# Kernel tuning notes

Hardware: AMD Instinct MI355X
Metric: run time of the kernel (lower is better)

## Reference

```python
import jax, jax.numpy as jnp
import numpy as np

GROUPS = 4
GROUP_SIZE = 64
NORMED = True


def setup_inputs() -> dict:
    key = jax.random.key(0)
    k1, k2 = jax.random.split(key)
    x = jax.random.normal(k1, (2, 4096, 4096), dtype=jnp.float32)
    # weight: [groups*group_out, group_in] = [4096, 1024], init std 0.02 as in torch
    weight = jax.random.normal(k2, (4096, 1024), dtype=jnp.float32) * 0.02
    return {"x": x, "weight": weight}


def reference(x, weight):
    if NORMED:
        # F.rms_norm with eps=None uses finfo(dtype).eps
        eps = jnp.finfo(x.dtype).eps
        x = x * jax.lax.rsqrt(jnp.mean(x * x, axis=-1, keepdims=True) + eps)

    # bf16 cast of weight (matches torch `.bfloat16()`), quantize in flat chunks of GROUP_SIZE
    w = weight.astype(jnp.bfloat16)
    w_g = w.reshape(-1, GROUP_SIZE)
    scale = jnp.clip(jnp.mean(jnp.abs(w_g), axis=-1, keepdims=True), 1e-8, None)
    q = jnp.clip(jnp.round(w_g / scale), -1.0, 1.0)
    # STE: forward value is q*scale, gradient flows through w
    w_ternary = w + jax.lax.stop_gradient((q * scale).reshape(w.shape) - w)

    group_in = weight.shape[1]
    group_out = weight.shape[0] // GROUPS
    w_grouped = w_ternary.reshape(GROUPS, group_out, group_in)

    bsz = x.shape[:-1]
    x_g = x.reshape(bsz + (GROUPS, group_in))
    # block-diagonal grouped matmul; promote bf16 weight to x dtype (exact upcast)
    out = jnp.einsum('...gi,goi->...go', x_g, w_grouped.astype(x.dtype))
    return out.reshape(bsz + (GROUPS * group_out,))
```

## Files before the change

kernel.cpp:

```cpp
#include <hip/hip_runtime.h>
#include <hip/hip_bf16.h>
#include <stdint.h>

__device__ __forceinline__ unsigned short f2bf(float f) {
    __hip_bfloat16 h = __float2bfloat16(f);
    return *reinterpret_cast<unsigned short*>(&h);
}
__device__ __forceinline__ float bf2f(unsigned short u) {
    __hip_bfloat16 h = *reinterpret_cast<__hip_bfloat16*>(&u);
    return __bfloat162float(h);
}

typedef __attribute__((ext_vector_type(8))) short bf16x8;
typedef __attribute__((ext_vector_type(4))) float f32x4;

__device__ __forceinline__ void async16(const void* g, void* l) {
    __builtin_amdgcn_global_load_lds(
        (const __attribute__((address_space(1))) unsigned int*)g,
        (__attribute__((address_space(3))) unsigned int*)l,
        16, 0, 0);
}

__global__ __launch_bounds__(256) void quant_kernel(const float* __restrict__ W,
                                                    unsigned short* __restrict__ Wq) {
    int idx = blockIdx.x * 256 + threadIdx.x;
    float wf = W[idx];
    float wbf = bf2f(f2bf(wf));
    float a = fabsf(wbf);
    float s = a;
    #pragma unroll
    for (int off = 32; off; off >>= 1) s += __shfl_xor(s, off, 64);
    float mean = s * (1.0f / 64.0f);
    float sf = bf2f(f2bf(mean));
    sf = fmaxf(sf, 1.0011718e-08f);
    float quot = bf2f(f2bf(wbf / sf));
    float q = rintf(quot);
    q = fminf(1.0f, fmaxf(-1.0f, q));
    float qs = q * sf;
    float d  = bf2f(f2bf(qs - wbf));
    Wq[idx] = f2bf(wbf + d);
}

__global__ __launch_bounds__(256) void norm_kernel(const float* __restrict__ X,
                                                   unsigned short* __restrict__ Xb) {
    __shared__ float red[4];
    const long long row = blockIdx.x;
    const float4* xr = (const float4*)(X + row * 4096);
    const int t = threadIdx.x;
    float4 v[4];
    float ss = 0.f;
    #pragma unroll
    for (int i = 0; i < 4; ++i) {
        v[i] = xr[i * 256 + t];
        ss += v[i].x * v[i].x + v[i].y * v[i].y + v[i].z * v[i].z + v[i].w * v[i].w;
    }
    #pragma unroll
    for (int off = 32; off; off >>= 1) ss += __shfl_xor(ss, off, 64);
    if ((t & 63) == 0) red[t >> 6] = ss;
    __syncthreads();
    const float tot = red[0] + red[1] + red[2] + red[3];
    const float scale = 1.0f / sqrtf(tot * (1.0f / 4096.0f) + 1.1920928955078125e-07f);
    ushort4* ob = (ushort4*)(Xb + row * 4096);
    #pragma unroll
    for (int i = 0; i < 4; ++i) {
        ushort4 o;
        o.x = f2bf(v[i].x * scale);
        o.y = f2bf(v[i].y * scale);
        o.z = f2bf(v[i].z * scale);
        o.w = f2bf(v[i].w * scale);
        ob[i * 256 + t] = o;
    }
}

__global__ __launch_bounds__(512, 2) void gemm_kernel(const unsigned short* __restrict__ Xb,
                                                      const unsigned short* __restrict__ Wq,
                                                      float* __restrict__ Out) {
    __shared__ unsigned short lsA[4][256 * 32];
    __shared__ unsigned short lsB[4][256 * 32];

    const int tid = threadIdx.x;
    const int lane = tid & 63;
    const int wv = tid >> 6;
    const int wr = wv >> 2;
    const int wc = wv & 3;

    const int bid = blockIdx.x;
    const int swz = (bid & 7) * 64 + (bid >> 3);
    const int bm0 = (swz & 31) * 256;
    const int bn0 = (swz >> 5) * 256;
    const int g = bn0 >> 10;

    const int srow = tid >> 2;
    const int cswz = (tid & 3) ^ ((tid >> 3) & 3);
    const unsigned short* pA0 = Xb + (long long)(bm0 + srow) * 4096 + g * 1024 + cswz * 8;
    const unsigned short* pA1 = pA0 + (long long)128 * 4096;
    const unsigned short* pB0 = Wq + (long long)(bn0 + srow) * 1024 + cswz * 8;
    const unsigned short* pB1 = pB0 + (long long)128 * 1024;
    const int ldst = tid * 8;

    const int cb = (lane >> 4) ^ ((lane >> 1) & 3);
    const int aOff = (wr * 128 + (lane & 15)) * 32 + cb * 8;
    const int bOff = (wc * 64 + (lane & 15)) * 32 + cb * 8;

    f32x4 acc[8][4];
    #pragma unroll
    for (int i = 0; i < 8; ++i)
        #pragma unroll
        for (int j = 0; j < 4; ++j) acc[i][j] = (f32x4){0.f, 0.f, 0.f, 0.f};

    const int T = 32;

    #pragma unroll
    for (int pt = 0; pt < 3; ++pt) {
        async16(pA0 + pt * 32, &lsA[pt][ldst]);
        async16(pA1 + pt * 32, &lsA[pt][ldst + 4096]);
        async16(pB0 + pt * 32, &lsB[pt][ldst]);
        async16(pB1 + pt * 32, &lsB[pt][ldst + 4096]);
    }
    asm volatile("s_waitcnt vmcnt(8)" ::: "memory");
    __builtin_amdgcn_s_barrier();

    for (int t = 0; t < T; ++t) {
        const unsigned short* sA = lsA[t & 3];
        const unsigned short* sB = lsB[t & 3];
        bf16x8 afr[4], bfr[4];

        #pragma unroll
        for (int ni = 0; ni < 4; ++ni) bfr[ni] = *(const bf16x8*)&sB[bOff + ni * 512];
        #pragma unroll
        for (int i = 0; i < 4; ++i) afr[i] = *(const bf16x8*)&sA[aOff + i * 512];
        if (t + 3 < T) {
            unsigned short* dA = lsA[(t + 3) & 3];
            async16(pA0 + (t + 3) * 32, dA + ldst);
            async16(pA1 + (t + 3) * 32, dA + ldst + 4096);
        }
        __builtin_amdgcn_s_barrier();
        __builtin_amdgcn_s_setprio(1);
        #pragma unroll
        for (int i = 0; i < 4; ++i)
            #pragma unroll
            for (int ni = 0; ni < 4; ++ni)
                acc[i][ni] = __builtin_amdgcn_mfma_f32_16x16x32_bf16(afr[i], bfr[ni], acc[i][ni], 0, 0, 0);
        __builtin_amdgcn_s_setprio(0);
        __builtin_amdgcn_s_barrier();

        #pragma unroll
        for (int i = 0; i < 4; ++i) afr[i] = *(const bf16x8*)&sA[aOff + (i + 4) * 512];
        if (t + 3 < T) {
            unsigned short* dB = lsB[(t + 3) & 3];
            async16(pB0 + (t + 3) * 32, dB + ldst);
            async16(pB1 + (t + 3) * 32, dB + ldst + 4096);
        }
        __builtin_amdgcn_s_barrier();
        __builtin_amdgcn_s_setprio(1);
        #pragma unroll
        for (int i = 0; i < 4; ++i)
            #pragma unroll
            for (int ni = 0; ni < 4; ++ni)
                acc[i + 4][ni] = __builtin_amdgcn_mfma_f32_16x16x32_bf16(afr[i], bfr[ni], acc[i + 4][ni], 0, 0, 0);
        __builtin_amdgcn_s_setprio(0);

        if (t < T - 3)       asm volatile("s_waitcnt vmcnt(8)" ::: "memory");
        else if (t == T - 3) asm volatile("s_waitcnt vmcnt(4)" ::: "memory");
        else if (t == T - 2) asm volatile("s_waitcnt vmcnt(0)" ::: "memory");
        __builtin_amdgcn_s_barrier();
    }

    #pragma unroll
    for (int mi = 0; mi < 8; ++mi) {
        #pragma unroll
        for (int ni = 0; ni < 4; ++ni) {
            const int col = bn0 + wc * 64 + ni * 16 + (lane & 15);
            const int rowb = bm0 + wr * 128 + mi * 16 + (lane >> 4) * 4;
            #pragma unroll
            for (int r = 0; r < 4; ++r)
                Out[(long long)(rowb + r) * 4096 + col] = acc[mi][ni][r];
        }
    }
}

extern "C" void kernel_launch(void* const* d_in, const int* in_sizes, int n_in,
                              void* d_out, int out_size, void* d_ws, size_t ws_size,
                              hipStream_t stream) {
    const float* x = (const float*)d_in[0];
    const float* w = (const float*)d_in[1];
    float* out = (float*)d_out;

    unsigned short* xb = (unsigned short*)d_ws;
    unsigned short* wq = xb + (size_t)8192 * 4096;

    quant_kernel<<<4096 * 1024 / 256, 256, 0, stream>>>(w, wq);
    norm_kernel<<<8192, 256, 0, stream>>>(x, xb);
    gemm_kernel<<<512, 512, 0, stream>>>(xb, wq, out);
}
```

Measured before the change: 336.1 us.

## Restructure GEMM main loop to BK=64 double-buffered ping-pong with quarter-tile MFMA phases

Replaces the 4-stage BK=32 LDS ring with two BK=64 buffers for A and B, staged in half-tiles. Each iteration now covers two k-tiles in eight MFMA quarter phases, and global prefetch is interleaved between them. The LDS swizzle moves to an 8-chunk XOR pattern to match the 64-wide rows. This cuts the loop-iteration and barrier overhead per unit of K and changes how loads overlap with compute, but adds more barriers per iteration and uses the full 128KB of LDS, which may limit occupancy.

```diff
diff --git a/kernel.cpp b/kernel.cpp
--- a/kernel.cpp
+++ b/kernel.cpp
@@ -75,11 +75,11 @@
 __global__ __launch_bounds__(512, 2) void gemm_kernel(const unsigned short* __restrict__ Xb,
                                                       const unsigned short* __restrict__ Wq,
                                                       float* __restrict__ Out) {
-    __shared__ unsigned short lsA[4][256 * 32];
-    __shared__ unsigned short lsB[4][256 * 32];
+    __shared__ __attribute__((aligned(16))) unsigned short ls[65536];
 
     const int tid = threadIdx.x;
     const int lane = tid & 63;
+    const int laneR = lane & 15;
     const int wv = tid >> 6;
     const int wr = wv >> 2;
     const int wc = wv & 3;
@@ -90,17 +90,41 @@
     const int bn0 = (swz >> 5) * 256;
     const int g = bn0 >> 10;
 
-    const int srow = tid >> 2;
-    const int cswz = (tid & 3) ^ ((tid >> 3) & 3);
-    const unsigned short* pA0 = Xb + (long long)(bm0 + srow) * 4096 + g * 1024 + cswz * 8;
-    const unsigned short* pA1 = pA0 + (long long)128 * 4096;
-    const unsigned short* pB0 = Wq + (long long)(bn0 + srow) * 1024 + cswz * 8;
-    const unsigned short* pB1 = pB0 + (long long)128 * 1024;
-    const int ldst = tid * 8;
-
-    const int cb = (lane >> 4) ^ ((lane >> 1) & 3);
-    const int aOff = (wr * 128 + (lane & 15)) * 32 + cb * 8;
-    const int bOff = (wc * 64 + (lane & 15)) * 32 + cb * 8;
+    const int srow = tid >> 3;
+    const int cswz8 = (((tid & 7) ^ (srow & 7)) << 3);
+    const unsigned short* aG = Xb + (long long)(bm0 + srow) * 4096 + g * 1024 + cswz8;
+    const unsigned short* bG = Wq + (long long)(bn0 + srow) * 1024 + cswz8;
+
+    const int col0 = (((lane >> 4) ^ (lane & 7)) << 3);
+    const int col1 = col0 ^ 32;
+
+    enum { A0 = 0, B0 = 16384, A1 = 32768, B1 = 49152 };
+
+    const int aRow = (wr * 128 + laneR) * 64;
+    const int bRow = (wc * 64 + laneR) * 64;
+
+#define STAGE_A(base, kt, h) do { \
+    async16(aG + ((long long)((h) * 128) * 4096 + (kt) * 64),      ls + (base) + (h) * 8192 + tid * 8); \
+    async16(aG + ((long long)((h) * 128 + 64) * 4096 + (kt) * 64), ls + (base) + (h) * 8192 + 4096 + tid * 8); \
+} while (0)
+#define STAGE_B(base, kt, h) do { \
+    async16(bG + ((long long)((h) * 128) * 1024 + (kt) * 64),      ls + (base) + (h) * 8192 + tid * 8); \
+    async16(bG + ((long long)((h) * 128 + 64) * 1024 + (kt) * 64), ls + (base) + (h) * 8192 + 4096 + tid * 8); \
+} while (0)
+#define LD(off) (*(const bf16x8*)(ls + (off)))
+#define MFMA_Q(MB, NB, bb) do { \
+    _Pragma("unroll") \
+    for (int mi = 0; mi < 4; ++mi) { \
+        _Pragma("unroll") \
+        for (int ni = 0; ni < 2; ++ni) { \
+            acc[(MB) + mi][(NB) + ni] = __builtin_amdgcn_mfma_f32_16x16x32_bf16(a[mi][0], bb[ni][0], acc[(MB) + mi][(NB) + ni], 0, 0, 0); \
+            acc[(MB) + mi][(NB) + ni] = __builtin_amdgcn_mfma_f32_16x16x32_bf16(a[mi][1], bb[ni][1], acc[(MB) + mi][(NB) + ni], 0, 0, 0); \
+        } \
+    } \
+} while (0)
+#define BAR() __builtin_amdgcn_s_barrier()
+#define PRIO1() __builtin_amdgcn_s_setprio(1)
+#define PRIO0() __builtin_amdgcn_s_setprio(0)
 
     f32x4 acc[8][4];
     #pragma unroll
@@ -108,75 +132,83 @@
         #pragma unroll
         for (int j = 0; j < 4; ++j) acc[i][j] = (f32x4){0.f, 0.f, 0.f, 0.f};
 
-    const int T = 32;
-
-    #pragma unroll
-    for (int pt = 0; pt < 3; ++pt) {
-        async16(pA0 + pt * 32, &lsA[pt][ldst]);
-        async16(pA1 + pt * 32, &lsA[pt][ldst + 4096]);
-        async16(pB0 + pt * 32, &lsB[pt][ldst]);
-        async16(pB1 + pt * 32, &lsB[pt][ldst + 4096]);
-    }
-    asm volatile("s_waitcnt vmcnt(8)" ::: "memory");
-    __builtin_amdgcn_s_barrier();
-
-    for (int t = 0; t < T; ++t) {
-        const unsigned short* sA = lsA[t & 3];
-        const unsigned short* sB = lsB[t & 3];
-        bf16x8 afr[4], bfr[4];
-
-        #pragma unroll
-        for (int ni = 0; ni < 4; ++ni) bfr[ni] = *(const bf16x8*)&sB[bOff + ni * 512];
-        #pragma unroll
-        for (int i = 0; i < 4; ++i) afr[i] = *(const bf16x8*)&sA[aOff + i * 512];
-        if (t + 3 < T) {
-            unsigned short* dA = lsA[(t + 3) & 3];
-            async16(pA0 + (t + 3) * 32, dA + ldst);
-            async16(pA1 + (t + 3) * 32, dA + ldst + 4096);
-        }
-        __builtin_amdgcn_s_barrier();
-        __builtin_amdgcn_s_setprio(1);
-        #pragma unroll
-        for (int i = 0; i < 4; ++i)
-            #pragma unroll
-            for (int ni = 0; ni < 4; ++ni)
-                acc[i][ni] = __builtin_amdgcn_mfma_f32_16x16x32_bf16(afr[i], bfr[ni], acc[i][ni], 0, 0, 0);
-        __builtin_amdgcn_s_setprio(0);
-        __builtin_amdgcn_s_barrier();
-
-        #pragma unroll
-        for (int i = 0; i < 4; ++i) afr[i] = *(const bf16x8*)&sA[aOff + (i + 4) * 512];
-        if (t + 3 < T) {
-            unsigned short* dB = lsB[(t + 3) & 3];
-            async16(pB0 + (t + 3) * 32, dB + ldst);
-            async16(pB1 + (t + 3) * 32, dB + ldst + 4096);
-        }
-        __builtin_amdgcn_s_barrier();
-        __builtin_amdgcn_s_setprio(1);
-        #pragma unroll
-        for (int i = 0; i < 4; ++i)
-            #pragma unroll
-            for (int ni = 0; ni < 4; ++ni)
-                acc[i + 4][ni] = __builtin_amdgcn_mfma_f32_16x16x32_bf16(afr[i], bfr[ni], acc[i + 4][ni], 0, 0, 0);
-        __builtin_amdgcn_s_setprio(0);
-
-        if (t < T - 3)       asm volatile("s_waitcnt vmcnt(8)" ::: "memory");
-        else if (t == T - 3) asm volatile("s_waitcnt vmcnt(4)" ::: "memory");
-        else if (t == T - 2) asm volatile("s_waitcnt vmcnt(0)" ::: "memory");
-        __builtin_amdgcn_s_barrier();
+    bf16x8 a[4][2], b[2][2], c[2][2];
+
+    STAGE_A(A0, 0, 0); STAGE_A(A0, 0, 1);
+    STAGE_B(B0, 0, 0); STAGE_B(B0, 0, 1);
+    STAGE_B(B1, 1, 0); STAGE_B(B1, 1, 1);
+    asm volatile("s_waitcnt vmcnt(4)" ::: "memory");
+    BAR();
+
+    #pragma unroll 1
+    for (int it = 0; it < 8; ++it) {
+        const int kt0 = it * 2, kt1 = kt0 + 1;
+        const bool pf = (it < 7);
+
+        #pragma unroll
+        for (int ni = 0; ni < 2; ++ni) { b[ni][0] = LD(B0 + bRow + ni * 1024 + col0); b[ni][1] = LD(B0 + bRow + ni * 1024 + col1); }
+        #pragma unroll
+        for (int mi = 0; mi < 4; ++mi) { a[mi][0] = LD(A0 + aRow + mi * 1024 + col0); a[mi][1] = LD(A0 + aRow + mi * 1024 + col1); }
+        STAGE_A(A1, kt1, 0);
+        BAR(); PRIO1(); MFMA_Q(0, 0, b); PRIO0(); BAR();
+
+        #pragma unroll
+        for (int ni = 0; ni < 2; ++ni) { c[ni][0] = LD(B0 + bRow + (ni + 2) * 1024 + col0); c[ni][1] = LD(B0 + bRow + (ni + 2) * 1024 + col1); }
+        STAGE_A(A1, kt1, 1);
+        BAR(); PRIO1(); MFMA_Q(0, 2, c); PRIO0(); BAR();
+
+        #pragma unroll
+        for (int mi = 0; mi < 4; ++mi) { a[mi][0] = LD(A0 + aRow + 4096 + mi * 1024 + col0); a[mi][1] = LD(A0 + aRow + 4096 + mi * 1024 + col1); }
+        if (pf) STAGE_B(B0, kt0 + 2, 0);
+        BAR(); PRIO1(); MFMA_Q(4, 0, b); PRIO0(); BAR();
+
+        if (pf) STAGE_B(B0, kt0 + 2, 1);
+        BAR(); PRIO1(); MFMA_Q(4, 2, c); PRIO0();
+        if (pf) { asm volatile("s_waitcnt vmcnt(4)" ::: "memory"); }
+        else    { asm volatile("s_waitcnt vmcnt(0)" ::: "memory"); }
+        BAR();
+
+        #pragma unroll
+        for (int ni = 0; ni < 2; ++ni) { b[ni][0] = LD(B1 + bRow + ni * 1024 + col0); b[ni][1] = LD(B1 + bRow + ni * 1024 + col1); }
+        #pragma unroll
+        for (int mi = 0; mi < 4; ++mi) { a[mi][0] = LD(A1 + aRow + mi * 1024 + col0); a[mi][1] = LD(A1 + aRow + mi * 1024 + col1); }
+        if (pf) STAGE_A(A0, kt0 + 2, 0);
+        BAR(); PRIO1(); MFMA_Q(0, 0, b); PRIO0(); BAR();
+
+        #pragma unroll
+        for (int ni = 0; ni < 2; ++ni) { c[ni][0] = LD(B1 + bRow + (ni + 2) * 1024 + col0); c[ni][1] = LD(B1 + bRow + (ni + 2) * 1024 + col1); }
+        if (pf) STAGE_A(A0, kt0 + 2, 1);
+        BAR(); PRIO1(); MFMA_Q(0, 2, c); PRIO0(); BAR();
+
+        #pragma unroll
+        for (int mi = 0; mi < 4; ++mi) { a[mi][0] = LD(A1 + aRow + 4096 + mi * 1024 + col0); a[mi][1] = LD(A1 + aRow + 4096 + mi * 1024 + col1); }
+        if (pf) STAGE_B(B1, kt1 + 2, 0);
+        BAR(); PRIO1(); MFMA_Q(4, 0, b); PRIO0(); BAR();
+
+        if (pf) STAGE_B(B1, kt1 + 2, 1);
+        BAR(); PRIO1(); MFMA_Q(4, 2, c); PRIO0();
+        if (pf) { asm volatile("s_waitcnt vmcnt(4)" ::: "memory"); }
+        BAR();
     }
 
     #pragma unroll
     for (int mi = 0; mi < 8; ++mi) {
         #pragma unroll
         for (int ni = 0; ni < 4; ++ni) {
-            const int col = bn0 + wc * 64 + ni * 16 + (lane & 15);
+            const int colo = bn0 + wc * 64 + ni * 16 + laneR;
             const int rowb = bm0 + wr * 128 + mi * 16 + (lane >> 4) * 4;
             #pragma unroll
             for (int r = 0; r < 4; ++r)
-                Out[(long long)(rowb + r) * 4096 + col] = acc[mi][ni][r];
+                Out[(long long)(rowb + r) * 4096 + colo] = acc[mi][ni][r];
         }
     }
+#undef STAGE_A
+#undef STAGE_B
+#undef LD
+#undef MFMA_Q
+#undef BAR
+#undef PRIO1
+#undef PRIO0
 }
 
 extern "C" void kernel_launch(void* const* d_in, const int* in_sizes, int n_in,
```

Measured after the change: 322.0 us. 4.2% less time.
